# Performance work log

Measured on AMD Instinct MI355X. Metric: run time of the kernel, lower is better.

The kernel has to match this reference:

```python
import jax, jax.numpy as jnp
import numpy as np

IN_F, OUT_F, N_TOK = 4096, 4096, 8192

def setup_inputs() -> dict:
    key = jax.random.key(0)
    k1, k2, k3 = jax.random.split(key, 3)
    x = jax.random.normal(k1, (N_TOK, IN_F), dtype=jnp.float32)
    scaler = jax.random.uniform(k2, (1,), dtype=jnp.float32)
    int8_weights = jax.random.randint(k3, (IN_F, OUT_F), -128, 128, dtype=jnp.int32)
    return {"x": x, "scaler": scaler, "int8_weights": int8_weights}

def reference(x, scaler, int8_weights):
    # dequantize int8 weights: fp_w = int8_w * scaler, then GEMM
    fp_weights = int8_weights.astype(x.dtype) * scaler  # [in, out]
    return jnp.matmul(x, fp_weights)  # [tokens, out]
```

## Files before the change

### kernel.cpp

```cpp
#include <hip/hip_runtime.h>

#define M_DIM 8192
#define N_DIM 4096
#define K_DIM 4096

typedef __attribute__((ext_vector_type(8))) __bf16 bf16x8;
typedef __attribute__((ext_vector_type(4))) float f32x4;
typedef __attribute__((ext_vector_type(8))) unsigned short u16x8;
typedef __attribute__((ext_vector_type(4))) unsigned short u16x4;

typedef const __attribute__((address_space(1))) unsigned int gu32_t;
typedef __attribute__((address_space(3))) unsigned int lu32_t;

static __device__ __forceinline__ unsigned short f2bf(float f) {
    union { float f; unsigned int u; } v; v.f = f;
    unsigned int u = v.u;
    return (unsigned short)((u + 0x7fffu + ((u >> 16) & 1u)) >> 16);
}

#define PREP_XBLOCKS 2048
#define PREP_WBLOCKS 2048

__global__ __launch_bounds__(256) void prep_kernel(const float* __restrict__ x,
                                                   unsigned short* __restrict__ xb,
                                                   const int* __restrict__ w,
                                                   unsigned short* __restrict__ wt) {
    __shared__ unsigned short t[64][68];
    const int tid = threadIdx.x;
    if (blockIdx.x < PREP_XBLOCKS) {
        const float4* xp = (const float4*)x;
        size_t g = (size_t)blockIdx.x * 256 + tid;
        const size_t stride = (size_t)PREP_XBLOCKS * 256;
#pragma unroll
        for (int it = 0; it < 8; ++it, g += stride) {
            float4 a = xp[2 * g], b = xp[2 * g + 1];
            u16x8 o;
            o[0] = f2bf(a.x); o[1] = f2bf(a.y); o[2] = f2bf(a.z); o[3] = f2bf(a.w);
            o[4] = f2bf(b.x); o[5] = f2bf(b.y); o[6] = f2bf(b.z); o[7] = f2bf(b.w);
            *(u16x8*)&xb[g * 8] = o;
        }
    } else {
        const int wb = blockIdx.x - PREP_XBLOCKS;
#pragma unroll
        for (int tt = 0; tt < 2; ++tt) {
            const int tile = wb * 2 + tt;
            const int n0 = (tile & 63) * 64;
            const int k0 = (tile >> 6) * 64;
#pragma unroll
            for (int p = 0; p < 4; ++p) {
                int r = p * 16 + (tid >> 4);
                int c = (tid & 15) * 4;
                int4 v = *(const int4*)&w[(size_t)(k0 + r) * N_DIM + n0 + c];
                u16x4 o4;
                o4[0] = f2bf((float)v.x); o4[1] = f2bf((float)v.y);
                o4[2] = f2bf((float)v.z); o4[3] = f2bf((float)v.w);
                *(u16x4*)&t[r][c] = o4;
            }
            __syncthreads();
#pragma unroll
            for (int p = 0; p < 2; ++p) {
                int idx = p * 256 + tid;
                int c  = idx >> 3;
                int r0 = (idx & 7) * 8;
                u16x8 o;
#pragma unroll
                for (int j = 0; j < 8; ++j) o[j] = t[r0 + j][c];
                *(u16x8*)&wt[(size_t)(n0 + c) * K_DIM + k0 + r0] = o;
            }
            __syncthreads();
        }
    }
}

__global__ __launch_bounds__(512, 2) void gemm256_kernel(const unsigned short* __restrict__ A,
                                                         const unsigned short* __restrict__ B,
                                                         const float* __restrict__ scaler,
                                                         float* __restrict__ C) {
    __shared__ unsigned short sm[65536];

    const int tid = threadIdx.x;

    const int bid  = blockIdx.x;
    const int sbid = (bid & 7) * 64 + (bid >> 3);
    const int m0   = (sbid & 31) * 256;
    const int n0   = (sbid >> 5) * 256;

    const int lane = tid & 63, wave = tid >> 6;
    const int lr   = lane & 15, quad = lane >> 4;
    const int wm   = wave >> 2, wn = wave & 3;

    const int d0 = tid * 16, d1 = d0 + 8192;
    const int l0 = d0 ^ ((((d0 >> 7) & 1) << 4) | (((d0 >> 8) & 1) << 5) | (((d0 >> 9) & 1) << 6));
    const int l1 = d1 ^ ((((d1 >> 7) & 1) << 4) | (((d1 >> 8) & 1) << 5) | (((d1 >> 9) & 1) << 6));
    const int srow0 = l0 >> 6, scol0 = (l0 & 63) >> 1;
    const int srow1 = l1 >> 6, scol1 = (l1 & 63) >> 1;
    const unsigned short* gA0 = A + (size_t)(m0 + srow0) * K_DIM + scol0;
    const unsigned short* gA1 = A + (size_t)(m0 + srow1) * K_DIM + scol1;
    const unsigned short* gB0 = B + (size_t)(n0 + srow0) * K_DIM + scol0;
    const unsigned short* gB1 = B + (size_t)(n0 + srow1) * K_DIM + scol1;
    char* smc = (char*)sm;

    const int amask = ((lr >> 1) & 7) << 4;
    const int afo = (((wm * 128 + lr) * 64) + quad * 16) ^ amask;
    const int bfo = (((wn * 64  + lr) * 64) + quad * 16) ^ amask;

    f32x4 acc[8][4];
#pragma unroll
    for (int i = 0; i < 8; ++i)
#pragma unroll
        for (int j = 0; j < 4; ++j) acc[i][j] = (f32x4){0.f, 0.f, 0.f, 0.f};

    bf16x8 af[4], bfr[4];

#define STAGE_A(buf, kh, kt) do { const int _ko = (kt) * 64 + (kh) * 32; \
    __builtin_amdgcn_global_load_lds((gu32_t*)(gA0 + _ko), (lu32_t*)(smc + ((buf)*4 + (kh)) * 16384 + d0), 16, 0, 0); \
    __builtin_amdgcn_global_load_lds((gu32_t*)(gA1 + _ko), (lu32_t*)(smc + ((buf)*4 + (kh)) * 16384 + d1), 16, 0, 0); \
} while (0)
#define STAGE_B(buf, kh, kt) do { const int _ko = (kt) * 64 + (kh) * 32; \
    __builtin_amdgcn_global_load_lds((gu32_t*)(gB0 + _ko), (lu32_t*)(smc + ((buf)*4 + 2 + (kh)) * 16384 + d0), 16, 0, 0); \
    __builtin_amdgcn_global_load_lds((gu32_t*)(gB1 + _ko), (lu32_t*)(smc + ((buf)*4 + 2 + (kh)) * 16384 + d1), 16, 0, 0); \
} while (0)
#define LOADA(buf, kh, ch) do { const char* _p = smc + ((buf)*4 + (kh)) * 16384 + (ch) * 4096 + afo; \
    _Pragma("unroll") for (int _mi = 0; _mi < 4; ++_mi) af[_mi] = *(const bf16x8*)(_p + _mi * 1024); \
} while (0)
#define LOADB(buf, kh) do { const char* _p = smc + ((buf)*4 + 2 + (kh)) * 16384 + bfo; \
    _Pragma("unroll") for (int _ni = 0; _ni < 4; ++_ni) bfr[_ni] = *(const bf16x8*)(_p + _ni * 1024); \
} while (0)
#define MFMA16(ch) do { __builtin_amdgcn_s_setprio(1); \
    _Pragma("unroll") for (int _mi = 0; _mi < 4; ++_mi) \
    _Pragma("unroll") for (int _ni = 0; _ni < 4; ++_ni) \
        acc[(ch)*4 + _mi][_ni] = __builtin_amdgcn_mfma_f32_16x16x32_bf16(af[_mi], bfr[_ni], acc[(ch)*4 + _mi][_ni], 0, 0, 0); \
    __builtin_amdgcn_s_setprio(0); \
} while (0)
#define BARRIER __builtin_amdgcn_s_barrier()
#define WAITL   asm volatile("s_waitcnt lgkmcnt(0)" ::: "memory")
#define WAITV4  asm volatile("s_waitcnt vmcnt(4)" ::: "memory")

    STAGE_A(0, 0, 0); STAGE_B(0, 0, 0);
    STAGE_A(0, 1, 0); STAGE_B(0, 1, 0);
    STAGE_A(1, 0, 1); STAGE_B(1, 0, 1);
    asm volatile("s_waitcnt vmcnt(0)" ::: "memory");
    BARRIER;

    for (int i = 0; i < K_DIM / 128; ++i) {
        const int t1 = 2 * i + 1;
        LOADA(0, 0, 0); LOADB(0, 0);
        STAGE_A(1, 1, t1);
        BARRIER; WAITL; MFMA16(0); BARRIER;
        LOADA(0, 0, 1);
        STAGE_B(1, 1, t1);
        BARRIER; WAITL; MFMA16(1); BARRIER;
        LOADA(0, 1, 1); LOADB(0, 1);
        STAGE_A(0, 0, (t1 + 1) & 63);
        BARRIER; WAITL; MFMA16(1); BARRIER;
        LOADA(0, 1, 0);
        STAGE_B(0, 0, (t1 + 1) & 63);
        BARRIER; WAITL; MFMA16(0); WAITV4; BARRIER;
        LOADA(1, 0, 0); LOADB(1, 0);
        STAGE_A(0, 1, (t1 + 1) & 63);
        BARRIER; WAITL; MFMA16(0); BARRIER;
        LOADA(1, 0, 1);
        STAGE_B(0, 1, (t1 + 1) & 63);
        BARRIER; WAITL; MFMA16(1); BARRIER;
        LOADA(1, 1, 1); LOADB(1, 1);
        STAGE_A(1, 0, (t1 + 2) & 63);
        BARRIER; WAITL; MFMA16(1); BARRIER;
        LOADA(1, 1, 0);
        STAGE_B(1, 0, (t1 + 2) & 63);
        BARRIER; WAITL; MFMA16(0); WAITV4; BARRIER;
    }
    asm volatile("s_waitcnt vmcnt(0)" ::: "memory");

    const float s = scaler[0];
#pragma unroll
    for (int mi = 0; mi < 8; ++mi)
#pragma unroll
        for (int ni = 0; ni < 4; ++ni) {
            const int row = m0 + wm * 128 + mi * 16 + quad * 4;
            const int col = n0 + wn * 64 + ni * 16 + lr;
            float* cp = C + (size_t)row * N_DIM + col;
#pragma unroll
            for (int r = 0; r < 4; ++r)
                cp[(size_t)r * N_DIM] = acc[mi][ni][r] * s;
        }

#undef STAGE_A
#undef STAGE_B
#undef LOADA
#undef LOADB
#undef MFMA16
#undef BARRIER
#undef WAITL
#undef WAITV4
}

extern "C" void kernel_launch(void* const* d_in, const int* in_sizes, int n_in,
                              void* d_out, int out_size, void* d_ws, size_t ws_size,
                              hipStream_t stream) {
    const float* x      = (const float*)d_in[0];
    const float* scaler = (const float*)d_in[1];
    const int*   w      = (const int*)d_in[2];
    float*       out    = (float*)d_out;

    unsigned short* xb = (unsigned short*)d_ws;
    unsigned short* wt = xb + (size_t)M_DIM * K_DIM;

    prep_kernel<<<PREP_XBLOCKS + PREP_WBLOCKS, 256, 0, stream>>>(x, xb, w, wt);
    gemm256_kernel<<<dim3((M_DIM / 256) * (N_DIM / 256)), 512, 0, stream>>>(xb, wt, scaler, out);
}
```

Baseline: 513.2 us.

## Split prep kernel, swizzle transpose LDS, remap GEMM tiles per XCD, add sched fences

The combined prep kernel is split into separate x-conversion and weight-transpose kernels, and the weight transpose tile in shared memory gets an XOR swizzle to reduce bank conflicts. The GEMM block-to-tile mapping is changed so each XCD works on a compact 8x8 patch of output tiles, which should improve L2 reuse of A and B panels. Scheduling barriers are inserted before each workgroup barrier so the compiler cannot move LDS reads and global-to-LDS loads across the pipeline phases. The extra kernel launch adds a little overhead, and the fences may limit the compiler's instruction interleaving.

```diff
diff --git a/kernel.cpp b/kernel.cpp
--- a/kernel.cpp
+++ b/kernel.cpp
@@ -21,54 +21,54 @@
 #define PREP_XBLOCKS 2048
 #define PREP_WBLOCKS 2048
 
-__global__ __launch_bounds__(256) void prep_kernel(const float* __restrict__ x,
-                                                   unsigned short* __restrict__ xb,
-                                                   const int* __restrict__ w,
-                                                   unsigned short* __restrict__ wt) {
+__global__ __launch_bounds__(256) void prep_x(const float* __restrict__ x,
+                                              unsigned short* __restrict__ xb) {
+    const int tid = threadIdx.x;
+    const float4* xp = (const float4*)x;
+    size_t g = (size_t)blockIdx.x * 256 + tid;
+    const size_t stride = (size_t)PREP_XBLOCKS * 256;
+#pragma unroll
+    for (int it = 0; it < 8; ++it, g += stride) {
+        float4 a = xp[2 * g], b = xp[2 * g + 1];
+        u16x8 o;
+        o[0] = f2bf(a.x); o[1] = f2bf(a.y); o[2] = f2bf(a.z); o[3] = f2bf(a.w);
+        o[4] = f2bf(b.x); o[5] = f2bf(b.y); o[6] = f2bf(b.z); o[7] = f2bf(b.w);
+        *(u16x8*)&xb[g * 8] = o;
+    }
+}
+
+__global__ __launch_bounds__(256) void prep_w(const int* __restrict__ w,
+                                              unsigned short* __restrict__ wt) {
     __shared__ unsigned short t[64][68];
     const int tid = threadIdx.x;
-    if (blockIdx.x < PREP_XBLOCKS) {
-        const float4* xp = (const float4*)x;
-        size_t g = (size_t)blockIdx.x * 256 + tid;
-        const size_t stride = (size_t)PREP_XBLOCKS * 256;
-#pragma unroll
-        for (int it = 0; it < 8; ++it, g += stride) {
-            float4 a = xp[2 * g], b = xp[2 * g + 1];
+#pragma unroll
+    for (int tt = 0; tt < 2; ++tt) {
+        const int tile = blockIdx.x * 2 + tt;
+        const int n0 = (tile & 63) * 64;
+        const int k0 = (tile >> 6) * 64;
+#pragma unroll
+        for (int p = 0; p < 4; ++p) {
+            int r = p * 16 + (tid >> 4);
+            int c = (tid & 15) * 4;
+            int4 v = *(const int4*)&w[(size_t)(k0 + r) * N_DIM + n0 + c];
+            u16x4 o4;
+            o4[0] = f2bf((float)v.x); o4[1] = f2bf((float)v.y);
+            o4[2] = f2bf((float)v.z); o4[3] = f2bf((float)v.w);
+            *(u16x4*)&t[r][c ^ (((r >> 3) & 7) << 2)] = o4;
+        }
+        __syncthreads();
+#pragma unroll
+        for (int p = 0; p < 2; ++p) {
+            int idx = p * 256 + tid;
+            int c  = idx >> 3;
+            int r0 = (idx & 7) * 8;
+            const int xr = (tid & 7) << 2;
             u16x8 o;
-            o[0] = f2bf(a.x); o[1] = f2bf(a.y); o[2] = f2bf(a.z); o[3] = f2bf(a.w);
-            o[4] = f2bf(b.x); o[5] = f2bf(b.y); o[6] = f2bf(b.z); o[7] = f2bf(b.w);
-            *(u16x8*)&xb[g * 8] = o;
+#pragma unroll
+            for (int j = 0; j < 8; ++j) o[j] = t[r0 + j][c ^ xr];
+            *(u16x8*)&wt[(size_t)(n0 + c) * K_DIM + k0 + r0] = o;
         }
-    } else {
-        const int wb = blockIdx.x - PREP_XBLOCKS;
-#pragma unroll
-        for (int tt = 0; tt < 2; ++tt) {
-            const int tile = wb * 2 + tt;
-            const int n0 = (tile & 63) * 64;
-            const int k0 = (tile >> 6) * 64;
-#pragma unroll
-            for (int p = 0; p < 4; ++p) {
-                int r = p * 16 + (tid >> 4);
-                int c = (tid & 15) * 4;
-                int4 v = *(const int4*)&w[(size_t)(k0 + r) * N_DIM + n0 + c];
-                u16x4 o4;
-                o4[0] = f2bf((float)v.x); o4[1] = f2bf((float)v.y);
-                o4[2] = f2bf((float)v.z); o4[3] = f2bf((float)v.w);
-                *(u16x4*)&t[r][c] = o4;
-            }
-            __syncthreads();
-#pragma unroll
-            for (int p = 0; p < 2; ++p) {
-                int idx = p * 256 + tid;
-                int c  = idx >> 3;
-                int r0 = (idx & 7) * 8;
-                u16x8 o;
-#pragma unroll
-                for (int j = 0; j < 8; ++j) o[j] = t[r0 + j][c];
-                *(u16x8*)&wt[(size_t)(n0 + c) * K_DIM + k0 + r0] = o;
-            }
-            __syncthreads();
-        }
+        __syncthreads();
     }
 }
 
@@ -80,10 +80,12 @@
 
     const int tid = threadIdx.x;
 
-    const int bid  = blockIdx.x;
-    const int sbid = (bid & 7) * 64 + (bid >> 3);
-    const int m0   = (sbid & 31) * 256;
-    const int n0   = (sbid >> 5) * 256;
+    const int bid = blockIdx.x;
+    const int xcd = bid & 7, j = bid >> 3;
+    const int mt  = (xcd >> 1) * 8 + (j & 7);
+    const int nt  = (xcd & 1) * 8 + (j >> 3);
+    const int m0  = mt * 256;
+    const int n0  = nt * 256;
 
     const int lane = tid & 63, wave = tid >> 6;
     const int lr   = lane & 15, quad = lane >> 4;
@@ -108,7 +110,7 @@
 #pragma unroll
     for (int i = 0; i < 8; ++i)
 #pragma unroll
-        for (int j = 0; j < 4; ++j) acc[i][j] = (f32x4){0.f, 0.f, 0.f, 0.f};
+        for (int j2 = 0; j2 < 4; ++j2) acc[i][j2] = (f32x4){0.f, 0.f, 0.f, 0.f};
 
     bf16x8 af[4], bfr[4];
 
@@ -132,6 +134,7 @@
         acc[(ch)*4 + _mi][_ni] = __builtin_amdgcn_mfma_f32_16x16x32_bf16(af[_mi], bfr[_ni], acc[(ch)*4 + _mi][_ni], 0, 0, 0); \
     __builtin_amdgcn_s_setprio(0); \
 } while (0)
+#define SFENCE  __builtin_amdgcn_sched_barrier(0)
 #define BARRIER __builtin_amdgcn_s_barrier()
 #define WAITL   asm volatile("s_waitcnt lgkmcnt(0)" ::: "memory")
 #define WAITV4  asm volatile("s_waitcnt vmcnt(4)" ::: "memory")
@@ -146,28 +149,28 @@
         const int t1 = 2 * i + 1;
         LOADA(0, 0, 0); LOADB(0, 0);
         STAGE_A(1, 1, t1);
-        BARRIER; WAITL; MFMA16(0); BARRIER;
+        SFENCE; BARRIER; WAITL; MFMA16(0); BARRIER;
         LOADA(0, 0, 1);
         STAGE_B(1, 1, t1);
-        BARRIER; WAITL; MFMA16(1); BARRIER;
+        SFENCE; BARRIER; WAITL; MFMA16(1); BARRIER;
         LOADA(0, 1, 1); LOADB(0, 1);
         STAGE_A(0, 0, (t1 + 1) & 63);
-        BARRIER; WAITL; MFMA16(1); BARRIER;
+        SFENCE; BARRIER; WAITL; MFMA16(1); BARRIER;
         LOADA(0, 1, 0);
         STAGE_B(0, 0, (t1 + 1) & 63);
-        BARRIER; WAITL; MFMA16(0); WAITV4; BARRIER;
+        SFENCE; BARRIER; WAITL; MFMA16(0); WAITV4; BARRIER;
         LOADA(1, 0, 0); LOADB(1, 0);
         STAGE_A(0, 1, (t1 + 1) & 63);
-        BARRIER; WAITL; MFMA16(0); BARRIER;
+        SFENCE; BARRIER; WAITL; MFMA16(0); BARRIER;
         LOADA(1, 0, 1);
         STAGE_B(0, 1, (t1 + 1) & 63);
-        BARRIER; WAITL; MFMA16(1); BARRIER;
+        SFENCE; BARRIER; WAITL; MFMA16(1); BARRIER;
         LOADA(1, 1, 1); LOADB(1, 1);
         STAGE_A(1, 0, (t1 + 2) & 63);
-        BARRIER; WAITL; MFMA16(1); BARRIER;
+        SFENCE; BARRIER; WAITL; MFMA16(1); BARRIER;
         LOADA(1, 1, 0);
         STAGE_B(1, 0, (t1 + 2) & 63);
-        BARRIER; WAITL; MFMA16(0); WAITV4; BARRIER;
+        SFENCE; BARRIER; WAITL; MFMA16(0); WAITV4; BARRIER;
     }
     asm volatile("s_waitcnt vmcnt(0)" ::: "memory");
 
@@ -189,6 +192,7 @@
 #undef LOADA
 #undef LOADB
 #undef MFMA16
+#undef SFENCE
 #undef BARRIER
 #undef WAITL
 #undef WAITV4
@@ -205,6 +209,7 @@
     unsigned short* xb = (unsigned short*)d_ws;
     unsigned short* wt = xb + (size_t)M_DIM * K_DIM;
 
-    prep_kernel<<<PREP_XBLOCKS + PREP_WBLOCKS, 256, 0, stream>>>(x, xb, w, wt);
+    prep_x<<<PREP_XBLOCKS, 256, 0, stream>>>(x, xb);
+    prep_w<<<PREP_WBLOCKS, 256, 0, stream>>>(w, wt);
     gemm256_kernel<<<dim3((M_DIM / 256) * (N_DIM / 256)), 512, 0, stream>>>(xb, wt, scaler, out);
 }
```

Result: faster. 492.0 us (-4.1%).
